# Performance work log

Hardware: AMD Instinct MI355X
Metric: run time of the kernel (lower is better)

The kernel has to match this reference:

```python
import jax, jax.numpy as jnp
import numpy as np

N = 4096
IN_DIM = 256
OUT_DIM = 256
H = 4
D = OUT_DIM // H  # per-head dim (concat=True)
ALPHA = 0.2
NEG_INF = -9e15


def setup_inputs() -> dict:
    key = jax.random.key(0)
    k1, k2, k3, k4, k5 = jax.random.split(key, 5)
    h = jax.random.normal(k1, (N, IN_DIM), dtype=jnp.float32)
    adj = jax.random.randint(k2, (N, N), 0, 2, dtype=jnp.int32)
    # Linear params (torch Linear: y = x @ W.T + b), xavier_uniform gain=1.414
    lim_w = 1.414 * np.sqrt(6.0 / (IN_DIM + H * D))
    W = jax.random.uniform(k3, (H * D, IN_DIM), dtype=jnp.float32, minval=-lim_w, maxval=lim_w)
    b = jnp.zeros((H * D,), dtype=jnp.float32)
    lim_a = 1.414 * np.sqrt(6.0 / (H + 2 * D))
    a = jax.random.uniform(k4, (H, 2 * D), dtype=jnp.float32, minval=-lim_a, maxval=lim_a)
    return {"h": h, "adj": adj, "W": W, "b": b, "a": a}


def reference(h, adj, W, b, a):
    # Wh: [N, H, D]
    Wh = (h @ W.T + b).reshape(N, H, D)
    # e_ij = leakyrelu(a . [Wh_i ; Wh_j]) decomposed into src/dst parts
    src = jnp.einsum('nhd,hd->nh', Wh, a[:, :D])   # [N, H], contribution of node i
    dst = jnp.einsum('nhd,hd->nh', Wh, a[:, D:])   # [N, H], contribution of node j
    e = src[:, None, :] + dst[None, :, :]          # [N, N, H]
    e = jax.nn.leaky_relu(e, negative_slope=ALPHA)
    # dense mask: non-edges get -9e15 (matches the original fill)
    att = jnp.where(adj[:, :, None] == 1, e, NEG_INF)
    att = jax.nn.softmax(att, axis=1)              # softmax over neighbors j per row i
    # dropout skipped (eval mode / deterministic reference)
    h_prime = jnp.einsum('ijh,jhd->ihd', att, Wh)  # [N, H, D]
    return h_prime.reshape(N, H * D)               # concat=True
```

## Files before the change

kernel.cpp:

```cpp
#include <hip/hip_runtime.h>

#define NN 4096
#define ALPHA 0.2f
#define FLTMAX 3.402823466e+38f
#define LOG2E 1.44269504088896340736f

typedef __attribute__((ext_vector_type(8))) short short8x;
typedef __attribute__((ext_vector_type(4))) float f32x4;
typedef __attribute__((ext_vector_type(4))) unsigned short ushort4x;
typedef unsigned long long u64;

__device__ __forceinline__ unsigned short f2bf(float f) {
  unsigned u = __float_as_uint(f);
  u += 0x7fffu + ((u >> 16) & 1u);
  return (unsigned short)(u >> 16);
}
__device__ __forceinline__ float bf2f(unsigned short s) {
  return __uint_as_float(((unsigned)s) << 16);
}
__device__ __forceinline__ unsigned fkey(float f) {
  unsigned b = __float_as_uint(f);
  return (b & 0x80000000u) ? ~b : (b | 0x80000000u);
}
__device__ __forceinline__ float funkey(unsigned k) {
  return __uint_as_float((k & 0x80000000u) ? (k & 0x7fffffffu) : ~k);
}

__global__ __launch_bounds__(256) void k0_prep(
    const float* __restrict__ W, unsigned short* __restrict__ Whi,
    unsigned short* __restrict__ Wlo, unsigned* __restrict__ dmaxkey)
{
  const int t = threadIdx.x;
  const int idx = blockIdx.x * 256 + t;
  float4 v = ((const float4*)W)[idx];
  const float vf[4] = {v.x, v.y, v.z, v.w};
  ushort4x hi, lo;
#pragma unroll
  for (int q = 0; q < 4; ++q) {
    unsigned short hb = f2bf(vf[q]);
    hi[q] = hb;
    lo[q] = f2bf(vf[q] - bf2f(hb));
  }
  ((ushort4x*)Whi)[idx] = hi;
  ((ushort4x*)Wlo)[idx] = lo;
  if (blockIdx.x == 0 && t < 4) dmaxkey[t] = 0x00800000u;
}

__global__ __launch_bounds__(256) void k1_mfma(
    const float* __restrict__ hin, const unsigned short* __restrict__ Whi,
    const unsigned short* __restrict__ Wlo, const float* __restrict__ bias,
    const float* __restrict__ av, unsigned short* __restrict__ WhT,
    float* __restrict__ srcv, float* __restrict__ dstv_soa,
    unsigned* __restrict__ dmaxkey)
{
  __shared__ float lds_s[4][16], lds_d[4][16];
  const int t = threadIdx.x;
  const int rb = blockIdx.x >> 2, h = blockIdx.x & 3;
  const int m0 = rb * 16;
  const int w = t >> 6, l = t & 63, r = l & 15, g = l >> 4;
  const int d = w * 16 + r;
  const int col = h * 64 + d;

  f32x4 acc = (f32x4){0.f, 0.f, 0.f, 0.f};
  const float* arow = hin + (size_t)(m0 + r) * 256 + g * 8;
  const unsigned short* bh = Whi + (size_t)col * 256 + g * 8;
  const unsigned short* bl = Wlo + (size_t)col * 256 + g * 8;

#pragma unroll
  for (int ks = 0; ks < 8; ++ks) {
    float4 a0 = *(const float4*)(arow + ks * 32);
    float4 a1 = *(const float4*)(arow + ks * 32 + 4);
    const float af[8] = {a0.x, a0.y, a0.z, a0.w, a1.x, a1.y, a1.z, a1.w};
    short8x ahi, alo;
#pragma unroll
    for (int j = 0; j < 8; ++j) {
      unsigned short hb = f2bf(af[j]);
      ahi[j] = (short)hb;
      alo[j] = (short)f2bf(af[j] - bf2f(hb));
    }
    short8x bhf = *(const short8x*)(bh + ks * 32);
    short8x blf = *(const short8x*)(bl + ks * 32);
    acc = __builtin_amdgcn_mfma_f32_16x16x32_bf16(ahi, bhf, acc, 0, 0, 0);
    acc = __builtin_amdgcn_mfma_f32_16x16x32_bf16(ahi, blf, acc, 0, 0, 0);
    acc = __builtin_amdgcn_mfma_f32_16x16x32_bf16(alo, bhf, acc, 0, 0, 0);
  }

  const float bc = bias[col];
  const float asrc = av[h * 128 + d];
  const float adst = av[h * 128 + 64 + d];
  float wv[4];
  ushort4x st;
#pragma unroll
  for (int q = 0; q < 4; ++q) {
    wv[q] = acc[q] + bc;
    st[q] = f2bf(wv[q]);
  }
  *(ushort4x*)(WhT + (size_t)col * NN + m0 + 4 * g) = st;

#pragma unroll
  for (int q = 0; q < 4; ++q) {
    float s = wv[q] * asrc, dd = wv[q] * adst;
#pragma unroll
    for (int off = 8; off >= 1; off >>= 1) {
      s += __shfl_xor(s, off);
      dd += __shfl_xor(dd, off);
    }
    if (r == 0) { lds_s[w][4 * g + q] = s * LOG2E; lds_d[w][4 * g + q] = dd * LOG2E; }
  }
  __syncthreads();
  if (t < 64) {
    const int row = t & 15;
    float s = lds_s[0][row] + lds_s[1][row] + lds_s[2][row] + lds_s[3][row];
    float dd = lds_d[0][row] + lds_d[1][row] + lds_d[2][row] + lds_d[3][row];
    if (t < 16) {
      srcv[(size_t)(m0 + row) * 4 + h] = s;
      dstv_soa[(size_t)h * NN + m0 + row] = dd;
    }
    float m = dd;
#pragma unroll
    for (int off = 1; off <= 32; off <<= 1) m = fmaxf(m, __shfl_xor(m, off));
    if (t == 0) atomicMax(dmaxkey + h, fkey(m));
  }
}

__global__ __launch_bounds__(256) void k2_mask(
    const int* __restrict__ adj, u64* __restrict__ bmask)
{
  const int t = threadIdx.x, wid = t >> 6, l = t & 63;
  const int row = blockIdx.x * 4 + wid;
  const int4* ap = (const int4*)(adj + (size_t)row * NN) + l;
  const int sh = 4 * (l & 15);
#pragma unroll
  for (int it = 0; it < 16; ++it) {
    int4 v = ap[(size_t)it * 64];
    unsigned nib = (v.x & 1) | ((v.y & 1) << 1) | ((v.z & 1) << 2) | ((v.w & 1) << 3);
    u64 w = (u64)nib << sh;
    w |= __shfl_xor(w, 1);
    w |= __shfl_xor(w, 2);
    w |= __shfl_xor(w, 4);
    w |= __shfl_xor(w, 8);
    if ((l & 15) == 0) bmask[(size_t)row * 64 + it * 4 + (l >> 4)] = w;
  }
}

__global__ __launch_bounds__(256, 4) void k3_mfma(
    const unsigned short* __restrict__ WhT, const float* __restrict__ srcv,
    const float* __restrict__ dstv_soa, const unsigned* __restrict__ dmaxkey,
    const u64* __restrict__ bmask,
    float* __restrict__ pacc, float* __restrict__ pden)
{
  __shared__ float lds_acc[2][64][33];
  __shared__ float lds_den[2][64][2];
  const int t = threadIdx.x;
  const int c  = blockIdx.x & 7;
  const int s  = c >> 1, hp = c & 1;
  const int rb = blockIdx.x >> 3;
  const int i0 = rb * 32;
  const int w = t >> 6, l = t & 63;
  const int hsel = w & 1, jh = w >> 1;
  const int h = hp * 2 + hsel;
  const int r = l & 15, g = l >> 4;
  const int j0 = s * 1024 + jh * 512;

  const float dmax = funkey(dmaxkey[h]);
  const float sr0 = srcv[(size_t)(i0 + r) * 4 + h];
  const float sr1 = srcv[(size_t)(i0 + 16 + r) * 4 + h];
  const float x0m = sr0 + dmax, x1m = sr1 + dmax;
  const float mr0 = fmaxf(x0m, ALPHA * x0m);
  const float mr1 = fmaxf(x1m, ALPHA * x1m);
  const float A0 = sr0 - mr0, C0 = ALPHA * sr0 - mr0;
  const float A1 = sr1 - mr1, C1 = ALPHA * sr1 - mr1;

  f32x4 acc[2][4];
#pragma unroll
  for (int m = 0; m < 2; ++m)
#pragma unroll
    for (int n = 0; n < 4; ++n) acc[m][n] = (f32x4){0.f, 0.f, 0.f, 0.f};
  float dacc0 = 0.f, dacc1 = 0.f;

  const unsigned short* whb = WhT + (size_t)(h * 64 + r) * NN + j0 + g * 8;
  const float* dpb = dstv_soa + (size_t)h * NN + j0 + g * 8;
  const u64* mb0 = bmask + (size_t)(i0 + r) * 64 + s * 16 + jh * 8;
  const u64* mb1 = bmask + (size_t)(i0 + 16 + r) * 64 + s * 16 + jh * 8;

  for (int tile = 0; tile < 8; ++tile) {
    const u64 wm0 = mb0[tile];
    const u64 wm1 = mb1[tile];
#pragma unroll
    for (int kt = 0; kt < 2; ++kt) {
      float4 da = *(const float4*)(dpb + tile * 64 + kt * 32);
      float4 db = *(const float4*)(dpb + tile * 64 + kt * 32 + 4);
      const unsigned bits0 = (unsigned)(wm0 >> (kt * 32 + g * 8)) & 0xffu;
      const unsigned bits1 = (unsigned)(wm1 >> (kt * 32 + g * 8)) & 0xffu;
      const float dvs[8] = {da.x, da.y, da.z, da.w, db.x, db.y, db.z, db.w};
      short8x a0, a1;
#pragma unroll
      for (int jj = 0; jj < 8; ++jj) {
        const float dv = dvs[jj];
        const float dva = ALPHA * dv;
        float e0 = fmaxf(A0 + dv, C0 + dva);
        e0 = ((bits0 >> jj) & 1u) ? e0 : -200.0f;
        unsigned pu0 = __float_as_uint(exp2f(e0));
        dacc0 += __uint_as_float(pu0 & 0xffff0000u);
        a0[jj] = (short)(pu0 >> 16);
        float e1 = fmaxf(A1 + dv, C1 + dva);
        e1 = ((bits1 >> jj) & 1u) ? e1 : -200.0f;
        unsigned pu1 = __float_as_uint(exp2f(e1));
        dacc1 += __uint_as_float(pu1 & 0xffff0000u);
        a1[jj] = (short)(pu1 >> 16);
      }
      short8x bfr[4];
#pragma unroll
      for (int n = 0; n < 4; ++n)
        bfr[n] = *(const short8x*)(whb + (size_t)(n * 16) * NN + tile * 64 + kt * 32);
#pragma unroll
      for (int n = 0; n < 4; ++n) {
        acc[0][n] = __builtin_amdgcn_mfma_f32_16x16x32_bf16(a0, bfr[n], acc[0][n], 0, 0, 0);
        acc[1][n] = __builtin_amdgcn_mfma_f32_16x16x32_bf16(a1, bfr[n], acc[1][n], 0, 0, 0);
      }
    }
  }

  if (jh == 1) {
#pragma unroll
    for (int m = 0; m < 2; ++m)
#pragma unroll
      for (int n = 0; n < 4; ++n)
#pragma unroll
        for (int q = 0; q < 4; ++q)
          lds_acc[hsel][l][m * 16 + n * 4 + q] = acc[m][n][q];
    lds_den[hsel][l][0] = dacc0;
    lds_den[hsel][l][1] = dacc1;
  }
  __syncthreads();
  if (jh == 0) {
#pragma unroll
    for (int m = 0; m < 2; ++m)
#pragma unroll
      for (int n = 0; n < 4; ++n)
#pragma unroll
        for (int q = 0; q < 4; ++q)
          acc[m][n][q] += lds_acc[hsel][l][m * 16 + n * 4 + q];
    dacc0 += lds_den[hsel][l][0];
    dacc1 += lds_den[hsel][l][1];
    dacc0 += __shfl_xor(dacc0, 16); dacc0 += __shfl_xor(dacc0, 32);
    dacc1 += __shfl_xor(dacc1, 16); dacc1 += __shfl_xor(dacc1, 32);
    if (l < 16) {
      pden[((size_t)s * NN + i0 + l) * 4 + h] = dacc0;
      pden[((size_t)s * NN + i0 + 16 + l) * 4 + h] = dacc1;
    }
#pragma unroll
    for (int m = 0; m < 2; ++m)
#pragma unroll
      for (int n = 0; n < 4; ++n)
#pragma unroll
        for (int q = 0; q < 4; ++q)
          pacc[((size_t)s * NN + i0 + 16 * m + g * 4 + q) * 256 + h * 64 + n * 16 + r] = acc[m][n][q];
  }
}

__global__ __launch_bounds__(256) void k4_combine(
    const float* __restrict__ pacc, const float* __restrict__ pden,
    float* __restrict__ out)
{
  const int t = threadIdx.x;
  const int i = blockIdx.x * 4 + (t >> 6);
  const int c4 = t & 63;
  const int h = c4 >> 4;
  const float4* pa = (const float4*)pacc;
  float4 num = {0.f, 0.f, 0.f, 0.f};
  float den = 0.f;
#pragma unroll
  for (int s = 0; s < 4; ++s) {
    float4 v = pa[((size_t)(s * NN + i)) * 64 + c4];
    num.x += v.x; num.y += v.y; num.z += v.z; num.w += v.w;
    den += pden[((size_t)s * NN + i) * 4 + h];
  }
  float inv = 1.f / den;
  float4 o = {num.x * inv, num.y * inv, num.z * inv, num.w * inv};
  ((float4*)out)[(size_t)i * 64 + c4] = o;
}

extern "C" void kernel_launch(void* const* d_in, const int* in_sizes, int n_in,
                              void* d_out, int out_size, void* d_ws, size_t ws_size,
                              hipStream_t stream) {
  const float* hin  = (const float*)d_in[0];
  const int*   adj  = (const int*)d_in[1];
  const float* W    = (const float*)d_in[2];
  const float* bias = (const float*)d_in[3];
  const float* av   = (const float*)d_in[4];
  float* out = (float*)d_out;

  char* ws = (char*)d_ws;
  unsigned short* WhT = (unsigned short*)(ws + 0x0);
  unsigned short* Whi = (unsigned short*)(ws + 0x200000);
  unsigned short* Wlo = (unsigned short*)(ws + 0x220000);
  float* srcv  = (float*)(ws + 0x240000);
  float* dstv  = (float*)(ws + 0x250000);
  unsigned* dmaxkey = (unsigned*)(ws + 0x260000);
  u64* bmask   = (u64*)(ws + 0x261000);
  float* pacc  = (float*)(ws + 0x461000);
  float* pden  = (float*)(ws + 0x1461000);

  k0_prep<<<64, 256, 0, stream>>>(W, Whi, Wlo, dmaxkey);
  k1_mfma<<<1024, 256, 0, stream>>>(hin, Whi, Wlo, bias, av, WhT, srcv, dstv, dmaxkey);
  k2_mask<<<1024, 256, 0, stream>>>(adj, bmask);
  k3_mfma<<<1024, 256, 0, stream>>>(WhT, srcv, dstv, dmaxkey, bmask, pacc, pden);
  k4_combine<<<NN / 4, 256, 0, stream>>>(pacc, pden, out);
}
```

Baseline: 184.5 us.

## Compute softmax denominators with MFMA against ones and pack bf16 via perm

The per-lane scalar denominator accumulation is replaced by an extra MFMA per k-step that multiplies the probability fragment by a vector of bf16 ones, which removes the VALU adds and the cross-lane shuffles from the epilogue. The exponential now uses the raw hardware exp2 instruction, two bf16 values are packed into one register with a perm instruction, and the ALPHA multiply-add is fused into an fma. The tile loop is unrolled by two. This shifts work from VALU to the matrix units at the cost of two extra MFMAs per step, and the fast exp2 skips the library's range handling.

```diff
diff --git a/kernel.cpp b/kernel.cpp
--- a/kernel.cpp
+++ b/kernel.cpp
@@ -8,6 +8,7 @@
 typedef __attribute__((ext_vector_type(8))) short short8x;
 typedef __attribute__((ext_vector_type(4))) float f32x4;
 typedef __attribute__((ext_vector_type(4))) unsigned short ushort4x;
+typedef __attribute__((ext_vector_type(4))) unsigned uint4x;
 typedef unsigned long long u64;
 
 __device__ __forceinline__ unsigned short f2bf(float f) {
@@ -24,6 +25,15 @@
 }
 __device__ __forceinline__ float funkey(unsigned k) {
   return __uint_as_float((k & 0x80000000u) ? (k & 0x7fffffffu) : ~k);
+}
+__device__ __forceinline__ float exp2v(float x) {
+#if __has_builtin(__builtin_amdgcn_exp2f)
+  return __builtin_amdgcn_exp2f(x);
+#else
+  float r;
+  asm("v_exp_f32 %0, %1" : "=v"(r) : "v"(x));
+  return r;
+#endif
 }
 
 __global__ __launch_bounds__(256) void k0_prep(
@@ -150,7 +160,7 @@
     float* __restrict__ pacc, float* __restrict__ pden)
 {
   __shared__ float lds_acc[2][64][33];
-  __shared__ float lds_den[2][64][2];
+  __shared__ float lds_dv[2][64][9];
   const int t = threadIdx.x;
   const int c  = blockIdx.x & 7;
   const int s  = c >> 1, hp = c & 1;
@@ -171,18 +181,24 @@
   const float A0 = sr0 - mr0, C0 = ALPHA * sr0 - mr0;
   const float A1 = sr1 - mr1, C1 = ALPHA * sr1 - mr1;
 
+  short8x ones;
+#pragma unroll
+  for (int i = 0; i < 8; ++i) ones[i] = (short)0x3F80;
+
   f32x4 acc[2][4];
 #pragma unroll
   for (int m = 0; m < 2; ++m)
 #pragma unroll
     for (int n = 0; n < 4; ++n) acc[m][n] = (f32x4){0.f, 0.f, 0.f, 0.f};
-  float dacc0 = 0.f, dacc1 = 0.f;
+  f32x4 accd0 = (f32x4){0.f, 0.f, 0.f, 0.f};
+  f32x4 accd1 = (f32x4){0.f, 0.f, 0.f, 0.f};
 
   const unsigned short* whb = WhT + (size_t)(h * 64 + r) * NN + j0 + g * 8;
   const float* dpb = dstv_soa + (size_t)h * NN + j0 + g * 8;
   const u64* mb0 = bmask + (size_t)(i0 + r) * 64 + s * 16 + jh * 8;
   const u64* mb1 = bmask + (size_t)(i0 + 16 + r) * 64 + s * 16 + jh * 8;
 
+#pragma unroll 2
   for (int tile = 0; tile < 8; ++tile) {
     const u64 wm0 = mb0[tile];
     const u64 wm1 = mb1[tile];
@@ -193,22 +209,27 @@
       const unsigned bits0 = (unsigned)(wm0 >> (kt * 32 + g * 8)) & 0xffu;
       const unsigned bits1 = (unsigned)(wm1 >> (kt * 32 + g * 8)) & 0xffu;
       const float dvs[8] = {da.x, da.y, da.z, da.w, db.x, db.y, db.z, db.w};
-      short8x a0, a1;
-#pragma unroll
-      for (int jj = 0; jj < 8; ++jj) {
-        const float dv = dvs[jj];
-        const float dva = ALPHA * dv;
-        float e0 = fmaxf(A0 + dv, C0 + dva);
-        e0 = ((bits0 >> jj) & 1u) ? e0 : -200.0f;
-        unsigned pu0 = __float_as_uint(exp2f(e0));
-        dacc0 += __uint_as_float(pu0 & 0xffff0000u);
-        a0[jj] = (short)(pu0 >> 16);
-        float e1 = fmaxf(A1 + dv, C1 + dva);
-        e1 = ((bits1 >> jj) & 1u) ? e1 : -200.0f;
-        unsigned pu1 = __float_as_uint(exp2f(e1));
-        dacc1 += __uint_as_float(pu1 & 0xffff0000u);
-        a1[jj] = (short)(pu1 >> 16);
+      uint4x pk0, pk1;
+#pragma unroll
+      for (int jp = 0; jp < 4; ++jp) {
+        const float dva_ = dvs[2 * jp], dvb_ = dvs[2 * jp + 1];
+        float e0a = fmaxf(A0 + dva_, fmaf(dva_, ALPHA, C0));
+        float e0b = fmaxf(A0 + dvb_, fmaf(dvb_, ALPHA, C0));
+        e0a = ((bits0 >> (2 * jp)) & 1u) ? e0a : -200.0f;
+        e0b = ((bits0 >> (2 * jp + 1)) & 1u) ? e0b : -200.0f;
+        unsigned pa0 = __float_as_uint(exp2v(e0a));
+        unsigned pb0 = __float_as_uint(exp2v(e0b));
+        pk0[jp] = __builtin_amdgcn_perm(pb0, pa0, 0x07060302);
+        float e1a = fmaxf(A1 + dva_, fmaf(dva_, ALPHA, C1));
+        float e1b = fmaxf(A1 + dvb_, fmaf(dvb_, ALPHA, C1));
+        e1a = ((bits1 >> (2 * jp)) & 1u) ? e1a : -200.0f;
+        e1b = ((bits1 >> (2 * jp + 1)) & 1u) ? e1b : -200.0f;
+        unsigned pa1 = __float_as_uint(exp2v(e1a));
+        unsigned pb1 = __float_as_uint(exp2v(e1b));
+        pk1[jp] = __builtin_amdgcn_perm(pb1, pa1, 0x07060302);
       }
+      const short8x a0 = __builtin_bit_cast(short8x, pk0);
+      const short8x a1 = __builtin_bit_cast(short8x, pk1);
       short8x bfr[4];
 #pragma unroll
       for (int n = 0; n < 4; ++n)
@@ -218,6 +239,8 @@
         acc[0][n] = __builtin_amdgcn_mfma_f32_16x16x32_bf16(a0, bfr[n], acc[0][n], 0, 0, 0);
         acc[1][n] = __builtin_amdgcn_mfma_f32_16x16x32_bf16(a1, bfr[n], acc[1][n], 0, 0, 0);
       }
+      accd0 = __builtin_amdgcn_mfma_f32_16x16x32_bf16(a0, ones, accd0, 0, 0, 0);
+      accd1 = __builtin_amdgcn_mfma_f32_16x16x32_bf16(a1, ones, accd1, 0, 0, 0);
     }
   }
 
@@ -229,8 +252,11 @@
 #pragma unroll
         for (int q = 0; q < 4; ++q)
           lds_acc[hsel][l][m * 16 + n * 4 + q] = acc[m][n][q];
-    lds_den[hsel][l][0] = dacc0;
-    lds_den[hsel][l][1] = dacc1;
+#pragma unroll
+    for (int q = 0; q < 4; ++q) {
+      lds_dv[hsel][l][q] = accd0[q];
+      lds_dv[hsel][l][4 + q] = accd1[q];
+    }
   }
   __syncthreads();
   if (jh == 0) {
@@ -241,13 +267,17 @@
 #pragma unroll
         for (int q = 0; q < 4; ++q)
           acc[m][n][q] += lds_acc[hsel][l][m * 16 + n * 4 + q];
-    dacc0 += lds_den[hsel][l][0];
-    dacc1 += lds_den[hsel][l][1];
-    dacc0 += __shfl_xor(dacc0, 16); dacc0 += __shfl_xor(dacc0, 32);
-    dacc1 += __shfl_xor(dacc1, 16); dacc1 += __shfl_xor(dacc1, 32);
-    if (l < 16) {
-      pden[((size_t)s * NN + i0 + l) * 4 + h] = dacc0;
-      pden[((size_t)s * NN + i0 + 16 + l) * 4 + h] = dacc1;
+#pragma unroll
+    for (int q = 0; q < 4; ++q) {
+      accd0[q] += lds_dv[hsel][l][q];
+      accd1[q] += lds_dv[hsel][l][4 + q];
+    }
+    if (r == 0) {
+#pragma unroll
+      for (int q = 0; q < 4; ++q) {
+        pden[((size_t)s * NN + i0 + 4 * g + q) * 4 + h] = accd0[q];
+        pden[((size_t)s * NN + i0 + 16 + 4 * g + q) * 4 + h] = accd1[q];
+      }
     }
 #pragma unroll
     for (int m = 0; m < 2; ++m)
```

Result: faster. 178.7 us (-3.2%).
